# Performance work log

Measured on AMD Instinct MI355X. Metric: run time of the kernel, lower is better.

## Reference

```python
import jax, jax.numpy as jnp
import numpy as np

N_NODES = 100000
N_EDGES = 1600000
HIDDEN = 64
N_MID = 3  # num_layers=5 -> 1 first + 3 middle + 1 last


def setup_inputs() -> dict:
    key = jax.random.key(0)
    ks = jax.random.split(key, 12)
    x = jax.random.normal(ks[0], (N_NODES, 1), dtype=jnp.float32)
    edge_index = jax.random.randint(ks[1], (2, N_EDGES), 0, N_NODES, dtype=jnp.int32)
    edge_weight = jax.random.uniform(ks[2], (N_EDGES,), dtype=jnp.float32)
    s0 = 1.0  # fan_in=1
    sh = 1.0 / np.sqrt(HIDDEN)
    Wrel0 = jax.random.normal(ks[3], (HIDDEN, 1), dtype=jnp.float32) * s0
    brel0 = jax.random.normal(ks[4], (HIDDEN,), dtype=jnp.float32) * s0
    Wroot0 = jax.random.normal(ks[5], (HIDDEN, 1), dtype=jnp.float32) * s0
    Wrel_mid = jax.random.normal(ks[6], (N_MID, HIDDEN, HIDDEN), dtype=jnp.float32) * sh
    brel_mid = jax.random.normal(ks[7], (N_MID, HIDDEN), dtype=jnp.float32) * sh
    Wroot_mid = jax.random.normal(ks[8], (N_MID, HIDDEN, HIDDEN), dtype=jnp.float32) * sh
    WrelL = jax.random.normal(ks[9], (1, HIDDEN), dtype=jnp.float32) * sh
    brelL = jax.random.normal(ks[10], (1,), dtype=jnp.float32) * sh
    WrootL = jax.random.normal(ks[11], (1, HIDDEN), dtype=jnp.float32) * sh
    return {"x": x, "edge_index": edge_index, "edge_weight": edge_weight,
            "Wrel0": Wrel0, "brel0": brel0, "Wroot0": Wroot0,
            "Wrel_mid": Wrel_mid, "brel_mid": brel_mid, "Wroot_mid": Wroot_mid,
            "WrelL": WrelL, "brelL": brelL, "WrootL": WrootL}


def reference(x, edge_index, edge_weight, Wrel0, brel0, Wroot0,
              Wrel_mid, brel_mid, Wroot_mid, WrelL, brelL, WrootL):
    src = edge_index[0]
    dst = edge_index[1]
    n = x.shape[0]

    def conv(h, Wrel, brel, Wroot):
        # PyG GraphConv(aggr='add'): lin_rel(sum_j w_ij * h_j) + lin_root(h_i)
        msg = h[src] * edge_weight[:, None]          # [E, C]
        agg = jax.ops.segment_sum(msg, dst, num_segments=n)  # [N, C]
        return agg @ Wrel.T + brel + h @ Wroot.T

    # dropout omitted (deterministic reference); relu after all but last layer
    h = jax.nn.relu(conv(x, Wrel0, brel0, Wroot0))
    for i in range(Wrel_mid.shape[0]):
        h = jax.nn.relu(conv(h, Wrel_mid[i], brel_mid[i], Wroot_mid[i]))
    return conv(h, WrelL, brelL, WrootL)  # [N, 1]
```

## Files before the change

kernel.cpp:

```cpp
#include <hip/hip_runtime.h>
#include <stdint.h>


#define NN 100000
#define NE 1600000
#define HID 64
#define NBKT 391
#define CAP 8192
#define PMAX (NBKT * CAP)
#define TILE 4096
#define EPT 16
#define NTILE ((NE + TILE - 1) / TILE)

typedef __attribute__((ext_vector_type(8))) short bf16x8;
typedef __attribute__((ext_vector_type(4))) float f32x4;
typedef __attribute__((ext_vector_type(2))) unsigned int u32x2;
typedef __attribute__((ext_vector_type(4))) unsigned int u32x4;

__device__ __forceinline__ uint32_t rne_bf16(float v) {
    uint32_t u = __float_as_uint(v);
    return (u + 0x7fffu + ((u >> 16) & 1u)) >> 16;
}


__global__ __launch_bounds__(256) void k_bpart(const int* __restrict__ src,
                                               const int* __restrict__ dst,
                                               const float* __restrict__ w,
                                               int* __restrict__ bcur,
                                               int2* __restrict__ bpairs) {
    __shared__ int  hcnt[NBKT];
    __shared__ int  hoff[NBKT];
    __shared__ int  hadj[NBKT];
    __shared__ int  sc0[512];
    __shared__ int  sc1[512];
    __shared__ int2 sT[TILE];
    __shared__ int  sAdj[TILE];
    int tile0 = blockIdx.x * TILE;
    int t = threadIdx.x;
    for (int i = t; i < NBKT; i += 256) hcnt[i] = 0;
    __syncthreads();

    int   pk[EPT];
    int   bk[EPT];
    float wv[EPT];
    #pragma unroll
    for (int k = 0; k < EPT; k++) {
        int e = tile0 + t + k * 256;
        if (e < NE) {
            int d = dst[e];
            int b = d >> 8;
            pk[k] = (src[e] << 8) | (d & 255);
            wv[k] = w[e];
            bk[k] = b;
            atomicAdd(&hcnt[b], 1);
        } else {
            bk[k] = -1;
        }
    }
    __syncthreads();

    sc0[t]       = (t < NBKT) ? hcnt[t] : 0;
    sc0[t + 256] = (t + 256 < NBKT) ? hcnt[t + 256] : 0;
    __syncthreads();
    int* cur = sc0;
    int* oth = sc1;
    for (int off = 1; off < 512; off <<= 1) {
        int v0 = cur[t]       + ((t       >= off) ? cur[t - off]       : 0);
        int v1 = cur[t + 256] + ((t + 256 >= off) ? cur[t + 256 - off] : 0);
        oth[t] = v0;
        oth[t + 256] = v1;
        __syncthreads();
        int* tmp = cur; cur = oth; oth = tmp;
    }
    for (int i = t; i < NBKT; i += 256) {
        int c = hcnt[i];
        int excl = cur[i] - c;
        hoff[i] = excl;
        int gbase = c ? atomicAdd(&bcur[i], c) : 0;
        hadj[i] = gbase - excl;
        hcnt[i] = 0;
    }
    __syncthreads();

    #pragma unroll
    for (int k = 0; k < EPT; k++) {
        if (bk[k] >= 0) {
            int b = bk[k];
            int pos = hoff[b] + atomicAdd(&hcnt[b], 1);
            sT[pos] = make_int2(pk[k], __float_as_int(wv[k]));
            sAdj[pos] = hadj[b];
        }
    }
    __syncthreads();

    int n = NE - tile0; if (n > TILE) n = TILE;
    for (int j = t; j < n; j += 256)
        bpairs[sAdj[j] + j] = sT[j];
}

__global__ __launch_bounds__(256) void k_bcsr(const int* __restrict__ bcur,
                                              const int2* __restrict__ bpairs,
                                              int* __restrict__ offs,
                                              int* __restrict__ ends,
                                              uint32_t* __restrict__ pairs) {
    __shared__ int2 sE[CAP];
    __shared__ int cnt[256];
    __shared__ int scn[256];
    __shared__ int cur[256];
    int k = blockIdx.x, t = threadIdx.x;
    int base = k * CAP;
    int scnt = bcur[k] - base;
    cnt[t] = 0;
    __syncthreads();
    for (int j = t; j < scnt; j += 256) {
        int2 q = bpairs[base + j];
        sE[j] = q;
        atomicAdd(&cnt[q.x & 255], 1);
    }
    __syncthreads();
    int v = cnt[t], acc = v;
    scn[t] = v;
    __syncthreads();
    for (int off = 1; off < 256; off <<= 1) {
        int u = (t >= off) ? scn[t - off] : 0;
        __syncthreads();
        acc += u;
        scn[t] = acc;
        __syncthreads();
    }
    int excl = acc - v;
    cur[t] = excl;
    int d = (k << 8) + t;
    if (d < NN) {
        offs[d] = base + excl;
        ends[d] = base + excl + v;
    }
    __syncthreads();
    for (int j = t; j < scnt; j += 256) {
        int2 q = sE[j];
        int pos = base + atomicAdd(&cur[q.x & 255], 1);
        uint32_t wb = rne_bf16(__int_as_float(q.y)) & 0x7fffu;
        pairs[pos] = (wb << 17) | (uint32_t)(q.x >> 8);
    }
}


__global__ __launch_bounds__(256) void k_wsplit(const float* __restrict__ Wrel_mid,
                                                const float* __restrict__ Wroot_mid,
                                                uint16_t* __restrict__ WgH,
                                                uint16_t* __restrict__ WgL,
                                                uint16_t* __restrict__ WrH,
                                                uint16_t* __restrict__ WrL,
                                                int* __restrict__ bcur) {
    int i = blockIdx.x * blockDim.x + threadIdx.x;
    if (i < NBKT) bcur[i] = i * CAP;
    if (i >= 3 * 4096) return;
    float a = Wrel_mid[i];
    uint32_t ah = rne_bf16(a);
    float al = a - __uint_as_float(ah << 16);
    WgH[i] = (uint16_t)ah;
    WgL[i] = (uint16_t)rne_bf16(al);
    float b = Wroot_mid[i];
    uint32_t bh = rne_bf16(b);
    float bl = b - __uint_as_float(bh << 16);
    WrH[i] = (uint16_t)bh;
    WrL[i] = (uint16_t)rne_bf16(bl);
}


__global__ __launch_bounds__(256) void k_l0pre(
        const int* __restrict__ offs, const int* __restrict__ ends,
        const uint32_t* __restrict__ pairs, const float* __restrict__ x,
        float2* __restrict__ AX) {
    int c = threadIdx.x & 63;
    int w = threadIdx.x >> 6;
    int blk16 = blockIdx.x * 16;
    #pragma unroll
    for (int t = 0; t < 4; t++) {
        int node = blk16 + w * 4 + t;
        int b = offs[node], e = ends[node];
        float pp = 0.f;
        for (int j = b + c; j < e; j += 64) {
            uint32_t r = pairs[j];
            pp += __uint_as_float((r >> 17) << 16) * x[r & 0x1ffffu];
        }
        for (int o = 32; o > 0; o >>= 1) pp += __shfl_down(pp, o, 64);
        if (c == 0) AX[node] = make_float2(pp, x[node]);
    }
}

#define TRRA(dst, off) \
    asm volatile("ds_read_b64_tr_b16 %0, %1 offset:" #off \
                 : "=v"(dst) : "v"(trbA))
#define TRRB(dst, off) \
    asm volatile("ds_read_b64_tr_b16 %0, %1 offset:" #off \
                 : "=v"(dst) : "v"(trbB))

__global__ __launch_bounds__(64, 4) void k_agg1(
        const int* __restrict__ offs, const int* __restrict__ ends,
        const uint32_t* __restrict__ pairs,
        const float2* __restrict__ AX,
        const float* __restrict__ Wrel0, const float* __restrict__ brel0,
        const float* __restrict__ Wroot0,
        const uint16_t* __restrict__ WgH, const uint16_t* __restrict__ WgL,
        const uint16_t* __restrict__ WrH, const uint16_t* __restrict__ WrL,
        const float* __restrict__ brel,
        uint16_t* __restrict__ Hout) {
    __shared__ __align__(128) char smem[4608];
    int c = threadIdx.x;
    int n0 = blockIdx.x * 16;
    int row = c & 15;
    int quad = c >> 4;
    int kq = quad * 8;

    int myNode = n0 + row;
    int blo = offs[myNode];
    int bhi = ends[myNode];
    uint32_t wid = (uint32_t)(bhi - blo);
    int start  = __builtin_amdgcn_readlane(blo, 0);
    int finish = __builtin_amdgcn_readlane(bhi, 15);

    float wrc[4], brc[4], woc[4];
    #pragma unroll
    for (int nb = 0; nb < 4; nb++) {
        int col = nb * 16 + row;
        wrc[nb] = Wrel0[col]; brc[nb] = brel0[col]; woc[nb] = Wroot0[col];
    }

    f32x4 acc16[4];
    #pragma unroll
    for (int nb = 0; nb < 4; nb++) acc16[nb] = f32x4{0.f, 0.f, 0.f, 0.f};

    float* abuf = (float*)smem;
    float* xbuf = (float*)(smem + 256);

    int j0 = start + c; if (j0 > PMAX - 1) j0 = PMAX - 1;
    uint32_t praw = pairs[j0];
    uint32_t p = (start + c < finish) ? praw : 0;

    for (int cb = start; cb < finish; cb += 64) {
        int jn = cb + 64 + c; if (jn > PMAX - 1) jn = PMAX - 1;
        uint32_t pr2 = pairs[jn];
        float2 ax = AX[p & 0x1ffffu];
        uint32_t mA[8], mB[8];
        int dbA = cb + kq - blo;
        int dbB = cb + 32 + kq - blo;
        #pragma unroll
        for (int q = 0; q < 8; q++) {
            uint32_t rq = (uint32_t)__builtin_amdgcn_ds_bpermute(
                (kq + q) * 4, (int)p);
            mA[q] = ((uint32_t)(dbA + q) < wid) ? (rq >> 17) : 0u;
        }
        #pragma unroll
        for (int q = 0; q < 8; q++) {
            uint32_t rq = (uint32_t)__builtin_amdgcn_ds_bpermute(
                (32 + kq + q) * 4, (int)p);
            mB[q] = ((uint32_t)(dbB + q) < wid) ? (rq >> 17) : 0u;
        }
        u32x4 aav = { mA[0] | (mA[1] << 16), mA[2] | (mA[3] << 16),
                      mA[4] | (mA[5] << 16), mA[6] | (mA[7] << 16) };
        u32x4 abv = { mB[0] | (mB[1] << 16), mB[2] | (mB[3] << 16),
                      mB[4] | (mB[5] << 16), mB[6] | (mB[7] << 16) };
        bf16x8 afA = __builtin_bit_cast(bf16x8, aav);
        bf16x8 afB = __builtin_bit_cast(bf16x8, abv);
        asm volatile("s_waitcnt vmcnt(0)" ::: "memory");
        abuf[c] = ax.x;
        xbuf[c] = ax.y;
        asm volatile("s_waitcnt lgkmcnt(0)" ::: "memory");
        __builtin_amdgcn_sched_barrier(0);
        #pragma unroll
        for (int s = 0; s < 2; s++) {
            f32x4 aL = *(const f32x4*)(smem + s * 128 + kq * 4);
            f32x4 aH = *(const f32x4*)(smem + s * 128 + kq * 4 + 16);
            f32x4 xL = *(const f32x4*)(smem + 256 + s * 128 + kq * 4);
            f32x4 xH = *(const f32x4*)(smem + 256 + s * 128 + kq * 4 + 16);
            asm volatile("s_waitcnt lgkmcnt(0)" ::: "memory");
            __builtin_amdgcn_sched_barrier(0);
            float ar[8], xr[8];
            #pragma unroll
            for (int q = 0; q < 4; q++) {
                ar[q] = aL[q]; ar[q + 4] = aH[q];
                xr[q] = xL[q]; xr[q + 4] = xH[q];
            }
            bf16x8 af = s ? afB : afA;
            #pragma unroll
            for (int nb = 0; nb < 4; nb++) {
                float wr = wrc[nb], br = brc[nb], wo = woc[nb];
                uint32_t bw[4];
                #pragma unroll
                for (int jj = 0; jj < 4; jj++) {
                    float h0 = fmaf(ar[2 * jj], wr, fmaf(xr[2 * jj], wo, br));
                    float h1 = fmaf(ar[2 * jj + 1], wr,
                                    fmaf(xr[2 * jj + 1], wo, br));
                    h0 = h0 > 0.f ? h0 : 0.f;
                    h1 = h1 > 0.f ? h1 : 0.f;
                    asm("v_cvt_pk_bf16_f32 %0, %1, %2"
                        : "=v"(bw[jj]) : "v"(h0), "v"(h1));
                }
                u32x4 bb = { bw[0], bw[1], bw[2], bw[3] };
                acc16[nb] = __builtin_amdgcn_mfma_f32_16x16x32_bf16(
                    af, __builtin_bit_cast(bf16x8, bb), acc16[nb], 0, 0, 0);
            }
        }
        p = (cb + 64 + c < finish) ? pr2 : 0;
    }

    float2 axs = AX[n0 + row];
    uint32_t e0[8], e1[8];
    #pragma unroll
    for (int q = 0; q < 8; q++) {
        int k0 = kq + q;
        float h = axs.x * Wrel0[k0] + brel0[k0] + axs.y * Wroot0[k0];
        h = h > 0.f ? h : 0.f;
        e0[q] = rne_bf16(h);
        int k1 = 32 + kq + q;
        float h2 = axs.x * Wrel0[k1] + brel0[k1] + axs.y * Wroot0[k1];
        h2 = h2 > 0.f ? h2 : 0.f;
        e1[q] = rne_bf16(h2);
    }
    u32x4 hv0 = { e0[0] | (e0[1] << 16), e0[2] | (e0[3] << 16),
                  e0[4] | (e0[5] << 16), e0[6] | (e0[7] << 16) };
    u32x4 hv1 = { e1[0] | (e1[1] << 16), e1[2] | (e1[3] << 16),
                  e1[4] | (e1[5] << 16), e1[6] | (e1[7] << 16) };
    bf16x8 hs0 = __builtin_bit_cast(bf16x8, hv0);
    bf16x8 hs1 = __builtin_bit_cast(bf16x8, hv1);

    uint32_t* sHw = (uint32_t*)smem;
    #pragma unroll
    for (int t = 0; t < 4; t++) {
        #pragma unroll
        for (int nb = 0; nb < 4; nb++) {
            uint32_t hb = rne_bf16(acc16[nb][t]);
            uint32_t pn2 = (uint32_t)__shfl_xor((int)hb, 1, 64);
            if (!(c & 1))
                sHw[(quad * 4 + t) * 36 + nb * 8 + (row >> 1)]
                    = hb | (pn2 << 16);
        }
    }
    asm volatile("s_waitcnt lgkmcnt(0)" ::: "memory");
    __builtin_amdgcn_sched_barrier(0);
    int kb = quad * 8;
    bf16x8 ah0 = *(const bf16x8*)&sHw[row * 36 + quad * 4];
    bf16x8 ah1 = *(const bf16x8*)&sHw[row * 36 + 16 + quad * 4];

    uint16_t* sO = (uint16_t*)(smem + 2304);
    #pragma unroll
    for (int ob = 0; ob < 4; ob++) {
        int oc = ob * 16 + row;
        float bias = brel[oc];
        f32x4 acc = {bias, bias, bias, bias};
        bf16x8 gh0 = *(const bf16x8*)&WgH[oc * 64 + kb];
        bf16x8 gh1 = *(const bf16x8*)&WgH[oc * 64 + 32 + kb];
        bf16x8 gl0 = *(const bf16x8*)&WgL[oc * 64 + kb];
        bf16x8 gl1 = *(const bf16x8*)&WgL[oc * 64 + 32 + kb];
        acc = __builtin_amdgcn_mfma_f32_16x16x32_bf16(ah0, gh0, acc, 0, 0, 0);
        acc = __builtin_amdgcn_mfma_f32_16x16x32_bf16(ah1, gh1, acc, 0, 0, 0);
        acc = __builtin_amdgcn_mfma_f32_16x16x32_bf16(ah0, gl0, acc, 0, 0, 0);
        acc = __builtin_amdgcn_mfma_f32_16x16x32_bf16(ah1, gl1, acc, 0, 0, 0);
        bf16x8 rh0 = *(const bf16x8*)&WrH[oc * 64 + kb];
        bf16x8 rh1 = *(const bf16x8*)&WrH[oc * 64 + 32 + kb];
        bf16x8 rl0 = *(const bf16x8*)&WrL[oc * 64 + kb];
        bf16x8 rl1 = *(const bf16x8*)&WrL[oc * 64 + 32 + kb];
        acc = __builtin_amdgcn_mfma_f32_16x16x32_bf16(hs0, rh0, acc, 0, 0, 0);
        acc = __builtin_amdgcn_mfma_f32_16x16x32_bf16(hs1, rh1, acc, 0, 0, 0);
        acc = __builtin_amdgcn_mfma_f32_16x16x32_bf16(hs0, rl0, acc, 0, 0, 0);
        acc = __builtin_amdgcn_mfma_f32_16x16x32_bf16(hs1, rl1, acc, 0, 0, 0);
        #pragma unroll
        for (int r = 0; r < 4; r++) {
            float v = acc[r] > 0.f ? acc[r] : 0.f;
            sO[(quad * 4 + r) * 68 + oc] = (uint16_t)rne_bf16(v);
        }
    }
    asm volatile("s_waitcnt lgkmcnt(0)" ::: "memory");
    __builtin_amdgcn_sched_barrier(0);
    const uint32_t* sOd = (const uint32_t*)sO;
    uint32_t* Hd = (uint32_t*)Hout;
    #pragma unroll
    for (int it = 0; it < 8; it++) {
        int idx = it * 64 + c;
        int nd = idx >> 5, col = idx & 31;
        Hd[(n0 + nd) * 32 + col] = sOd[nd * 34 + col];
    }
}

template <bool LAST>
__global__ __launch_bounds__(64, 5) void k_aggfused(
        const int* __restrict__ offs, const int* __restrict__ ends,
        const uint32_t* __restrict__ pairs,
        const uint16_t* __restrict__ Hb,
        const uint16_t* __restrict__ WgH, const uint16_t* __restrict__ WgL,
        const uint16_t* __restrict__ WrH, const uint16_t* __restrict__ WrL,
        const float* __restrict__ brel,
        uint16_t* __restrict__ Hout,
        const float* __restrict__ WrelL, const float* __restrict__ WrootL,
        float* __restrict__ sarr, float* __restrict__ rarr) {
    __shared__ __align__(128) char smem[8192];
    int c = threadIdx.x;
    int n0 = blockIdx.x * 16;

    int myNode = n0 + (c & 15);
    int blo = offs[myNode];
    int bhi = ends[myNode];
    uint32_t wid = (uint32_t)(bhi - blo);
    int start  = __builtin_amdgcn_readlane(blo, 0);
    int finish = __builtin_amdgcn_readlane(bhi, 15);

    int kq = (c >> 4) * 8;
    int eprm  = ((c >> 5) << 2) | ((c >> 1) & 3);
    int lbyte = ((c >> 3) & 3) * 32 + (c & 1) * 16;
    char* stg = smem;
    uint32_t stgOff = (uint32_t)(uintptr_t)
        (__attribute__((address_space(3))) char*)stg;
    uint32_t trbA = stgOff + ((uint32_t)(c >> 4) << 10)
                          + ((uint32_t)(c & 15) << 3);
    uint32_t trbB = trbA + 4096;

    f32x4 acc16[4];
    #pragma unroll
    for (int nb = 0; nb < 4; nb++) acc16[nb] = f32x4{0.f, 0.f, 0.f, 0.f};

    const char* gbase = (const char*)Hb;
    int j0 = start + c; if (j0 > PMAX - 1) j0 = PMAX - 1;
    uint32_t praw = pairs[j0];
    uint32_t p = (start + c < finish) ? praw : 0;

    for (int cb = start; cb < finish; cb += 64) {
        int jn = cb + 64 + c; if (jn > PMAX - 1) jn = PMAX - 1;
        uint32_t pr2 = pairs[jn];
        #pragma unroll
        for (int i = 0; i < 4; i++) {
            uint32_t r = (uint32_t)__builtin_amdgcn_ds_bpermute(
                (eprm + i * 8) * 4, (int)p);
            uint32_t voff = ((r & 0x1ffffu) << 7) + (uint32_t)lbyte;
            __builtin_amdgcn_global_load_lds(
                (const __attribute__((address_space(1))) void*)(gbase + voff),
                (__attribute__((address_space(3))) void*)(stg + i * 1024),
                16, 0, 0);
        }
        #pragma unroll
        for (int i = 0; i < 4; i++) {
            uint32_t r = (uint32_t)__builtin_amdgcn_ds_bpermute(
                (32 + eprm + i * 8) * 4, (int)p);
            uint32_t voff = ((r & 0x1ffffu) << 7) + (uint32_t)lbyte;
            __builtin_amdgcn_global_load_lds(
                (const __attribute__((address_space(1))) void*)(gbase + voff),
                (__attribute__((address_space(3))) void*)(stg + 4096 + i * 1024),
                16, 0, 0);
        }
        uint32_t mA[8], mB[8];
        int dbA = cb + kq - blo;
        int dbB = cb + 32 + kq - blo;
        #pragma unroll
        for (int q = 0; q < 8; q++) {
            uint32_t rq = (uint32_t)__builtin_amdgcn_ds_bpermute(
                (kq + q) * 4, (int)p);
            mA[q] = ((uint32_t)(dbA + q) < wid) ? (rq >> 17) : 0u;
        }
        #pragma unroll
        for (int q = 0; q < 8; q++) {
            uint32_t rq = (uint32_t)__builtin_amdgcn_ds_bpermute(
                (32 + kq + q) * 4, (int)p);
            mB[q] = ((uint32_t)(dbB + q) < wid) ? (rq >> 17) : 0u;
        }
        u32x4 aav = { mA[0] | (mA[1] << 16), mA[2] | (mA[3] << 16),
                      mA[4] | (mA[5] << 16), mA[6] | (mA[7] << 16) };
        u32x4 abv = { mB[0] | (mB[1] << 16), mB[2] | (mB[3] << 16),
                      mB[4] | (mB[5] << 16), mB[6] | (mB[7] << 16) };
        bf16x8 afA = __builtin_bit_cast(bf16x8, aav);
        bf16x8 afB = __builtin_bit_cast(bf16x8, abv);
        asm volatile("s_waitcnt vmcnt(4)" ::: "memory");
        {
            u32x2 tb0, tb1, tb2, tb3, tb4, tb5, tb6, tb7;
            TRRA(tb0, 0);   TRRA(tb1, 512);
            TRRA(tb2, 128); TRRA(tb3, 640);
            TRRA(tb4, 256); TRRA(tb5, 768);
            TRRA(tb6, 384); TRRA(tb7, 896);
            asm volatile("s_waitcnt lgkmcnt(0)" ::: "memory");
            __builtin_amdgcn_sched_barrier(0);
            u32x4 bb0 = { tb0.x, tb0.y, tb1.x, tb1.y };
            acc16[0] = __builtin_amdgcn_mfma_f32_16x16x32_bf16(
                afA, __builtin_bit_cast(bf16x8, bb0), acc16[0], 0, 0, 0);
            u32x4 bb1 = { tb2.x, tb2.y, tb3.x, tb3.y };
            acc16[1] = __builtin_amdgcn_mfma_f32_16x16x32_bf16(
                afA, __builtin_bit_cast(bf16x8, bb1), acc16[1], 0, 0, 0);
            u32x4 bb2 = { tb4.x, tb4.y, tb5.x, tb5.y };
            acc16[2] = __builtin_amdgcn_mfma_f32_16x16x32_bf16(
                afA, __builtin_bit_cast(bf16x8, bb2), acc16[2], 0, 0, 0);
            u32x4 bb3 = { tb6.x, tb6.y, tb7.x, tb7.y };
            acc16[3] = __builtin_amdgcn_mfma_f32_16x16x32_bf16(
                afA, __builtin_bit_cast(bf16x8, bb3), acc16[3], 0, 0, 0);
        }
        asm volatile("s_waitcnt vmcnt(0)" ::: "memory");
        {
            u32x2 tb0, tb1, tb2, tb3, tb4, tb5, tb6, tb7;
            TRRB(tb0, 0);   TRRB(tb1, 512);
            TRRB(tb2, 128); TRRB(tb3, 640);
            TRRB(tb4, 256); TRRB(tb5, 768);
            TRRB(tb6, 384); TRRB(tb7, 896);
            asm volatile("s_waitcnt lgkmcnt(0)" ::: "memory");
            __builtin_amdgcn_sched_barrier(0);
            u32x4 bb0 = { tb0.x, tb0.y, tb1.x, tb1.y };
            acc16[0] = __builtin_amdgcn_mfma_f32_16x16x32_bf16(
                afB, __builtin_bit_cast(bf16x8, bb0), acc16[0], 0, 0, 0);
            u32x4 bb1 = { tb2.x, tb2.y, tb3.x, tb3.y };
            acc16[1] = __builtin_amdgcn_mfma_f32_16x16x32_bf16(
                afB, __builtin_bit_cast(bf16x8, bb1), acc16[1], 0, 0, 0);
            u32x4 bb2 = { tb4.x, tb4.y, tb5.x, tb5.y };
            acc16[2] = __builtin_amdgcn_mfma_f32_16x16x32_bf16(
                afB, __builtin_bit_cast(bf16x8, bb2), acc16[2], 0, 0, 0);
            u32x4 bb3 = { tb6.x, tb6.y, tb7.x, tb7.y };
            acc16[3] = __builtin_amdgcn_mfma_f32_16x16x32_bf16(
                afB, __builtin_bit_cast(bf16x8, bb3), acc16[3], 0, 0, 0);
        }
        p = (cb + 64 + c < finish) ? pr2 : 0;
    }
    asm volatile("s_waitcnt vmcnt(0)" ::: "memory");

    int row = c & 15;
    int quad = c >> 4;
    int kb = quad * 8;
    bf16x8 hs0 = *(const bf16x8*)&Hb[(n0 + row) * 64 + kb];
    bf16x8 hs1 = *(const bf16x8*)&Hb[(n0 + row) * 64 + 32 + kb];
    uint32_t* sHw = (uint32_t*)smem;
    #pragma unroll
    for (int t = 0; t < 4; t++) {
        #pragma unroll
        for (int nb = 0; nb < 4; nb++) {
            uint32_t hb = rne_bf16(acc16[nb][t]);
            uint32_t pn2 = (uint32_t)__shfl_xor((int)hb, 1, 64);
            if (!(c & 1))
                sHw[(quad * 4 + t) * 36 + nb * 8 + (row >> 1)]
                    = hb | (pn2 << 16);
        }
    }
    asm volatile("s_waitcnt lgkmcnt(0)" ::: "memory");
    __builtin_amdgcn_sched_barrier(0);
    bf16x8 ah0 = *(const bf16x8*)&sHw[row * 36 + quad * 4];
    bf16x8 ah1 = *(const bf16x8*)&sHw[row * 36 + 16 + quad * 4];

    if (!LAST) {
        uint16_t* sO = (uint16_t*)(smem + 2304);
        #pragma unroll
        for (int ob = 0; ob < 4; ob++) {
            int oc = ob * 16 + row;
            float bias = brel[oc];
            f32x4 acc = {bias, bias, bias, bias};
            bf16x8 gh0 = *(const bf16x8*)&WgH[oc * 64 + kb];
            bf16x8 gh1 = *(const bf16x8*)&WgH[oc * 64 + 32 + kb];
            bf16x8 gl0 = *(const bf16x8*)&WgL[oc * 64 + kb];
            bf16x8 gl1 = *(const bf16x8*)&WgL[oc * 64 + 32 + kb];
            acc = __builtin_amdgcn_mfma_f32_16x16x32_bf16(ah0, gh0, acc, 0, 0, 0);
            acc = __builtin_amdgcn_mfma_f32_16x16x32_bf16(ah1, gh1, acc, 0, 0, 0);
            acc = __builtin_amdgcn_mfma_f32_16x16x32_bf16(ah0, gl0, acc, 0, 0, 0);
            acc = __builtin_amdgcn_mfma_f32_16x16x32_bf16(ah1, gl1, acc, 0, 0, 0);
            bf16x8 rh0 = *(const bf16x8*)&WrH[oc * 64 + kb];
            bf16x8 rh1 = *(const bf16x8*)&WrH[oc * 64 + 32 + kb];
            bf16x8 rl0 = *(const bf16x8*)&WrL[oc * 64 + kb];
            bf16x8 rl1 = *(const bf16x8*)&WrL[oc * 64 + 32 + kb];
            acc = __builtin_amdgcn_mfma_f32_16x16x32_bf16(hs0, rh0, acc, 0, 0, 0);
            acc = __builtin_amdgcn_mfma_f32_16x16x32_bf16(hs1, rh1, acc, 0, 0, 0);
            acc = __builtin_amdgcn_mfma_f32_16x16x32_bf16(hs0, rl0, acc, 0, 0, 0);
            acc = __builtin_amdgcn_mfma_f32_16x16x32_bf16(hs1, rl1, acc, 0, 0, 0);
            #pragma unroll
            for (int r = 0; r < 4; r++) {
                float v = acc[r] > 0.f ? acc[r] : 0.f;
                sO[(quad * 4 + r) * 68 + oc] = (uint16_t)rne_bf16(v);
            }
        }
        asm volatile("s_waitcnt lgkmcnt(0)" ::: "memory");
        __builtin_amdgcn_sched_barrier(0);
        const uint32_t* sOd = (const uint32_t*)sO;
        uint32_t* Hd = (uint32_t*)Hout;
        #pragma unroll
        for (int it = 0; it < 8; it++) {
            int idx = it * 64 + c;
            int nd = idx >> 5, col = idx & 31;
            Hd[(n0 + nd) * 32 + col] = sOd[nd * 34 + col];
        }
    } else {
        float pa[4] = {0.f, 0.f, 0.f, 0.f};
        float pr[4] = {0.f, 0.f, 0.f, 0.f};
        #pragma unroll
        for (int ob = 0; ob < 4; ob++) {
            int oc = ob * 16 + row;
            float bias = brel[oc];
            f32x4 acc = {bias, bias, bias, bias};
            bf16x8 gh0 = *(const bf16x8*)&WgH[oc * 64 + kb];
            bf16x8 gh1 = *(const bf16x8*)&WgH[oc * 64 + 32 + kb];
            bf16x8 gl0 = *(const bf16x8*)&WgL[oc * 64 + kb];
            bf16x8 gl1 = *(const bf16x8*)&WgL[oc * 64 + 32 + kb];
            acc = __builtin_amdgcn_mfma_f32_16x16x32_bf16(ah0, gh0, acc, 0, 0, 0);
            acc = __builtin_amdgcn_mfma_f32_16x16x32_bf16(ah1, gh1, acc, 0, 0, 0);
            acc = __builtin_amdgcn_mfma_f32_16x16x32_bf16(ah0, gl0, acc, 0, 0, 0);
            acc = __builtin_amdgcn_mfma_f32_16x16x32_bf16(ah1, gl1, acc, 0, 0, 0);
            bf16x8 rh0 = *(const bf16x8*)&WrH[oc * 64 + kb];
            bf16x8 rh1 = *(const bf16x8*)&WrH[oc * 64 + 32 + kb];
            bf16x8 rl0 = *(const bf16x8*)&WrL[oc * 64 + kb];
            bf16x8 rl1 = *(const bf16x8*)&WrL[oc * 64 + 32 + kb];
            acc = __builtin_amdgcn_mfma_f32_16x16x32_bf16(hs0, rh0, acc, 0, 0, 0);
            acc = __builtin_amdgcn_mfma_f32_16x16x32_bf16(hs1, rh1, acc, 0, 0, 0);
            acc = __builtin_amdgcn_mfma_f32_16x16x32_bf16(hs0, rl0, acc, 0, 0, 0);
            acc = __builtin_amdgcn_mfma_f32_16x16x32_bf16(hs1, rl1, acc, 0, 0, 0);
            float wlc = WrelL[oc], woc = WrootL[oc];
            #pragma unroll
            for (int r = 0; r < 4; r++) {
                float v = acc[r] > 0.f ? acc[r] : 0.f;
                pa[r] += v * wlc;
                pr[r] += v * woc;
            }
        }
        #pragma unroll
        for (int r = 0; r < 4; r++) {
            #pragma unroll
            for (int o = 8; o > 0; o >>= 1) {
                pa[r] += __shfl_down(pa[r], o, 16);
                pr[r] += __shfl_down(pr[r], o, 16);
            }
            if (row == 0) {
                int node = n0 + quad * 4 + r;
                sarr[node] = pa[r];
                rarr[node] = pr[r];
            }
        }
    }
}

__global__ __launch_bounds__(256) void k_last(
        const int* __restrict__ offs, const int* __restrict__ ends,
        const uint32_t* __restrict__ pairs,
        const float* __restrict__ sarr, const float* __restrict__ rarr,
        const float* __restrict__ brelL, float* __restrict__ out) {
    int c = threadIdx.x & 63;
    int w = threadIdx.x >> 6;
    int blk16 = blockIdx.x * 16;
    float b0 = brelL[0];
    #pragma unroll
    for (int t = 0; t < 4; t++) {
        int node = blk16 + w * 4 + t;
        int b = offs[node], e = ends[node];
        float pp = 0.f;
        for (int j = b + c; j < e; j += 64) {
            uint32_t r = pairs[j];
            pp += __uint_as_float((r >> 17) << 16) * sarr[r & 0x1ffffu];
        }
        #pragma unroll
        for (int o = 32; o > 0; o >>= 1) pp += __shfl_down(pp, o, 64);
        if (c == 0) out[node] = pp + rarr[node] + b0;
    }
}

extern "C" void kernel_launch(void* const* d_in, const int* in_sizes, int n_in,
                              void* d_out, int out_size, void* d_ws, size_t ws_size,
                              hipStream_t stream) {
    const float* x        = (const float*)d_in[0];
    const int*   ei       = (const int*)d_in[1];
    const float* ew       = (const float*)d_in[2];
    const float* Wrel0    = (const float*)d_in[3];
    const float* brel0    = (const float*)d_in[4];
    const float* Wroot0   = (const float*)d_in[5];
    const float* Wrel_mid = (const float*)d_in[6];
    const float* brel_mid = (const float*)d_in[7];
    const float* Wroot_mid= (const float*)d_in[8];
    const float* WrelL    = (const float*)d_in[9];
    const float* brelL    = (const float*)d_in[10];
    const float* WrootL   = (const float*)d_in[11];
    float* out = (float*)d_out;

    const int* src  = ei;
    const int* dstp = ei + NE;

    char* w = (char*)d_ws;
    size_t o = 0;
    auto alloc = [&](size_t b) -> void* {
        void* r = (void*)(w + o);
        o += (b + 255) & ~(size_t)255;
        return r;
    };
    int*      offs  = (int*)alloc((size_t)NN * 4);
    int*      ends  = (int*)alloc((size_t)NN * 4);
    int*      bcur  = (int*)alloc((size_t)NBKT * 4);
    uint16_t* WgH   = (uint16_t*)alloc((size_t)3 * 4096 * 2);
    uint16_t* WgL   = (uint16_t*)alloc((size_t)3 * 4096 * 2);
    uint16_t* WrH   = (uint16_t*)alloc((size_t)3 * 4096 * 2);
    uint16_t* WrL   = (uint16_t*)alloc((size_t)3 * 4096 * 2);
    float*    sarr  = (float*)alloc((size_t)NN * 4);
    float*    rarr  = (float*)alloc((size_t)NN * 4);
    float2*   AX    = (float2*)alloc((size_t)NN * 8);
    uint32_t* pairs = (uint32_t*)alloc((size_t)NBKT * CAP * 4);
    uint16_t* HbA   = (uint16_t*)alloc((size_t)NN * HID * 2);
    uint16_t* HbB   = (uint16_t*)alloc((size_t)NN * HID * 2);
    uint16_t* spare = (uint16_t*)alloc((size_t)NN * HID * 2);
    (void)spare;
    int2*  bpairs = (int2*)HbB;

    k_wsplit<<<(3 * 4096 + 255) / 256, 256, 0, stream>>>(
        Wrel_mid, Wroot_mid, WgH, WgL, WrH, WrL, bcur);

    k_bpart<<<NTILE, 256, 0, stream>>>(src, dstp, ew, bcur, bpairs);
    k_bcsr<<<NBKT, 256, 0, stream>>>(bcur, bpairs, offs, ends, pairs);

    k_l0pre<<<NN / 16, 256, 0, stream>>>(offs, ends, pairs, x, AX);

    int nagg = NN / 16;
    k_agg1<<<nagg, 64, 0, stream>>>(
        offs, ends, pairs, AX, Wrel0, brel0, Wroot0,
        WgH, WgL, WrH, WrL, brel_mid, HbB);
    k_aggfused<false><<<nagg, 64, 0, stream>>>(
        offs, ends, pairs, HbB,
        WgH + 4096, WgL + 4096, WrH + 4096, WrL + 4096, brel_mid + HID,
        HbA, WrelL, WrootL, sarr, rarr);
    k_aggfused<true><<<nagg, 64, 0, stream>>>(
        offs, ends, pairs, HbA,
        WgH + 2 * 4096, WgL + 2 * 4096, WrH + 2 * 4096, WrL + 2 * 4096,
        brel_mid + 2 * HID,
        HbB, WrelL, WrootL, sarr, rarr);

    k_last<<<NN / 16, 256, 0, stream>>>(offs, ends, pairs, sarr, rarr, brelL, out);
}
```

Baseline: 280.7 us.

## Fuse layer-0 scalar aggregation into CSR build and narrow last-layer gather

Removes the separate k_l0pre kernel and computes the layer-0 weighted sum of x per destination node inside k_bcsr, using LDS float atomics while the bucket edges are first loaded. This drops one launch and a second pass over pairs and offsets. Separately, k_last now gives each node 16 lanes instead of a full 64-lane wave processed four times in sequence, which suits the average degree of about 16. The LDS atomic accumulation changes the order of the float summation, and k_bcsr picks up extra random reads of x.

Result: faster. 264.1 us, median of 2 (-5.9%).

```diff
diff --git a/kernel.cpp b/kernel.cpp
--- a/kernel.cpp
+++ b/kernel.cpp
@@ -100,22 +100,29 @@
 
 __global__ __launch_bounds__(256) void k_bcsr(const int* __restrict__ bcur,
                                               const int2* __restrict__ bpairs,
+                                              const float* __restrict__ x,
                                               int* __restrict__ offs,
                                               int* __restrict__ ends,
-                                              uint32_t* __restrict__ pairs) {
+                                              uint32_t* __restrict__ pairs,
+                                              float2* __restrict__ AX) {
     __shared__ int2 sE[CAP];
     __shared__ int cnt[256];
     __shared__ int scn[256];
     __shared__ int cur[256];
+    __shared__ float aggx[256];
     int k = blockIdx.x, t = threadIdx.x;
     int base = k * CAP;
     int scnt = bcur[k] - base;
     cnt[t] = 0;
+    aggx[t] = 0.f;
     __syncthreads();
     for (int j = t; j < scnt; j += 256) {
         int2 q = bpairs[base + j];
         sE[j] = q;
         atomicAdd(&cnt[q.x & 255], 1);
+        uint32_t wb = rne_bf16(__int_as_float(q.y)) & 0x7fffu;
+        float wf = __uint_as_float(wb << 16);
+        atomicAdd(&aggx[q.x & 255], wf * x[q.x >> 8]);
     }
     __syncthreads();
     int v = cnt[t], acc = v;
@@ -134,6 +141,7 @@
     if (d < NN) {
         offs[d] = base + excl;
         ends[d] = base + excl + v;
+        AX[d] = make_float2(aggx[t], x[d]);
     }
     __syncthreads();
     for (int j = t; j < scnt; j += 256) {
@@ -167,27 +175,6 @@
     WrL[i] = (uint16_t)rne_bf16(bl);
 }
 
-
-__global__ __launch_bounds__(256) void k_l0pre(
-        const int* __restrict__ offs, const int* __restrict__ ends,
-        const uint32_t* __restrict__ pairs, const float* __restrict__ x,
-        float2* __restrict__ AX) {
-    int c = threadIdx.x & 63;
-    int w = threadIdx.x >> 6;
-    int blk16 = blockIdx.x * 16;
-    #pragma unroll
-    for (int t = 0; t < 4; t++) {
-        int node = blk16 + w * 4 + t;
-        int b = offs[node], e = ends[node];
-        float pp = 0.f;
-        for (int j = b + c; j < e; j += 64) {
-            uint32_t r = pairs[j];
-            pp += __uint_as_float((r >> 17) << 16) * x[r & 0x1ffffu];
-        }
-        for (int o = 32; o > 0; o >>= 1) pp += __shfl_down(pp, o, 64);
-        if (c == 0) AX[node] = make_float2(pp, x[node]);
-    }
-}
 
 #define TRRA(dst, off) \
     asm volatile("ds_read_b64_tr_b16 %0, %1 offset:" #off \
@@ -632,21 +619,19 @@
         const float* __restrict__ brelL, float* __restrict__ out) {
     int c = threadIdx.x & 63;
     int w = threadIdx.x >> 6;
-    int blk16 = blockIdx.x * 16;
+    int g = c >> 4;
+    int l = c & 15;
+    int node = blockIdx.x * 16 + w * 4 + g;
     float b0 = brelL[0];
-    #pragma unroll
-    for (int t = 0; t < 4; t++) {
-        int node = blk16 + w * 4 + t;
-        int b = offs[node], e = ends[node];
-        float pp = 0.f;
-        for (int j = b + c; j < e; j += 64) {
-            uint32_t r = pairs[j];
-            pp += __uint_as_float((r >> 17) << 16) * sarr[r & 0x1ffffu];
-        }
-        #pragma unroll
-        for (int o = 32; o > 0; o >>= 1) pp += __shfl_down(pp, o, 64);
-        if (c == 0) out[node] = pp + rarr[node] + b0;
-    }
+    int b = offs[node], e = ends[node];
+    float pp = 0.f;
+    for (int j = b + l; j < e; j += 16) {
+        uint32_t r = pairs[j];
+        pp += __uint_as_float((r >> 17) << 16) * sarr[r & 0x1ffffu];
+    }
+    #pragma unroll
+    for (int o = 8; o > 0; o >>= 1) pp += __shfl_down(pp, o, 16);
+    if (l == 0) out[node] = pp + rarr[node] + b0;
 }
 
 extern "C" void kernel_launch(void* const* d_in, const int* in_sizes, int n_in,
@@ -697,9 +682,7 @@
         Wrel_mid, Wroot_mid, WgH, WgL, WrH, WrL, bcur);
 
     k_bpart<<<NTILE, 256, 0, stream>>>(src, dstp, ew, bcur, bpairs);
-    k_bcsr<<<NBKT, 256, 0, stream>>>(bcur, bpairs, offs, ends, pairs);
-
-    k_l0pre<<<NN / 16, 256, 0, stream>>>(offs, ends, pairs, x, AX);
+    k_bcsr<<<NBKT, 256, 0, stream>>>(bcur, bpairs, x, offs, ends, pairs, AX);
 
     int nagg = NN / 16;
     k_agg1<<<nagg, 64, 0, stream>>>(
```
